# Kernel tuning notes

Measured on AMD Instinct MI355X. Metric: run time of the kernel, lower is better.

Reference implementation:

```python
import jax, jax.numpy as jnp
import numpy as np

B, S, D, H = 2, 2048, 1024, 16
HD = D // H
SCALE = float(np.sqrt(HD))


def setup_inputs() -> dict:
    key = jax.random.key(0)
    k_x, k_wqkv, k_bqkv, k_wo, k_bo = jax.random.split(key, 5)
    std = 1.0 / np.sqrt(D)
    x = jax.random.normal(k_x, (B, S, D), dtype=jnp.float32)
    mask = jnp.tril(jnp.ones((S, S), dtype=jnp.int32))[None, None]  # (1,1,S,S) causal
    W_qkv = jax.random.normal(k_wqkv, (D, 3 * D), dtype=jnp.float32) * std
    b_qkv = jax.random.normal(k_bqkv, (3 * D,), dtype=jnp.float32) * std
    W_o = jax.random.normal(k_wo, (D, D), dtype=jnp.float32) * std
    b_o = jax.random.normal(k_bo, (D,), dtype=jnp.float32) * std
    return {"x": x, "W_qkv": W_qkv, "b_qkv": b_qkv, "W_o": W_o, "b_o": b_o, "mask": mask}


def reference(x, W_qkv, b_qkv, W_o, b_o, mask):
    # fused QKV projection: (B,S,3D) -> (3,B,H,S,HD)
    qkv = x @ W_qkv + b_qkv
    qkv = qkv.reshape(B, S, 3, H, HD).transpose(2, 0, 3, 1, 4)
    Q, K, V = qkv[0], qkv[1], qkv[2]
    # scaled dot-product attention with explicit mask
    scores = jnp.einsum('bhqd,bhkd->bhqk', Q, K) / SCALE
    scores = jnp.where(mask == 0, -jnp.inf, scores)
    attn = jax.nn.softmax(scores, axis=-1)  # dropout p=0.0 -> identity
    context = jnp.einsum('bhqk,bhkd->bhqd', attn, V)
    context = context.transpose(0, 2, 1, 3).reshape(B, S, D)
    return context @ W_o + b_o
```

## Files before the change

### kernel.cpp

```cpp
#include <hip/hip_runtime.h>
#include <hip/hip_bf16.h>
#include <stdint.h>

#define DEV __device__ __forceinline__

typedef __bf16 bf16x8 __attribute__((ext_vector_type(8)));
typedef float f32x4 __attribute__((ext_vector_type(4)));
typedef float f32x16 __attribute__((ext_vector_type(16)));
typedef unsigned short ushort8 __attribute__((ext_vector_type(8)));

DEV uint16_t f2bf(float f) {
  uint32_t u = __float_as_uint(f);
  u += 0x7fffu + ((u >> 16) & 1u);
  return (uint16_t)(u >> 16);
}

DEV float exp2r(float x) {
  float r;
  asm("v_exp_f32 %0, %1" : "=v"(r) : "v"(x));
  return r;
}

DEV void gload_lds16(const void* g, void* l) {
  __builtin_amdgcn_global_load_lds(
      (const __attribute__((address_space(1))) void*)g,
      (__attribute__((address_space(3))) void*)l, 16, 0, 0);
}

DEV void swap32u(uint32_t& a, uint32_t& b) {
#if defined(__has_builtin) && __has_builtin(__builtin_amdgcn_permlane32_swap)
  auto r = __builtin_amdgcn_permlane32_swap(a, b, false, false);
  a = (uint32_t)r[0];
  b = (uint32_t)r[1];
#else
  uint32_t as = __shfl_xor(a, 32), bs = __shfl_xor(b, 32);
  uint32_t na = (threadIdx.x & 32) ? bs : a;
  uint32_t nb = (threadIdx.x & 32) ? b : as;
  a = na; b = nb;
#endif
}
DEV void swap32f(float& a, float& b) {
  uint32_t ua = __float_as_uint(a), ub = __float_as_uint(b);
  swap32u(ua, ub);
  a = __uint_as_float(ua); b = __uint_as_float(ub);
}

__global__ __launch_bounds__(256) void k_prep(const float* __restrict__ W0,
                                              uint16_t* __restrict__ WT0,
                                              const float* __restrict__ W1,
                                              uint16_t* __restrict__ WT1,
                                              const float* __restrict__ X,
                                              uint16_t* __restrict__ Xb) {
  const int z = blockIdx.z;
  const int tid = threadIdx.x;
  if (z == 2) {
    const int nt4 = 1048576, stride = 48 * 16 * 256;
    int base = (blockIdx.y * 48 + blockIdx.x) * 256 + tid;
    for (int i = base; i < nt4; i += stride) {
      float4 v = *reinterpret_cast<const float4*>(X + (size_t)i * 4);
      ushort4 o = { f2bf(v.x), f2bf(v.y), f2bf(v.z), f2bf(v.w) };
      *reinterpret_cast<ushort4*>(Xb + (size_t)i * 4) = o;
    }
    return;
  }
  if (z == 1 && blockIdx.x >= 16) return;
  const float* W = z ? W1 : W0;
  uint16_t* WT = z ? WT1 : WT0;
  const int K = 1024, N = z ? 1024 : 3072;
  __shared__ float t[64][65];
  int n0 = blockIdx.x * 64, k0 = blockIdx.y * 64;
  int r = tid >> 4, c4 = (tid & 15) * 4;
#pragma unroll
  for (int p = 0; p < 4; ++p) {
    int kr = p * 16 + r;
    float4 v = *reinterpret_cast<const float4*>(W + (size_t)(k0 + kr) * N + n0 + c4);
    t[kr][c4] = v.x; t[kr][c4 + 1] = v.y; t[kr][c4 + 2] = v.z; t[kr][c4 + 3] = v.w;
  }
  __syncthreads();
#pragma unroll
  for (int p = 0; p < 4; ++p) {
    int nr = p * 16 + r;
    ushort4 o = { f2bf(t[c4][nr]), f2bf(t[c4 + 1][nr]), f2bf(t[c4 + 2][nr]), f2bf(t[c4 + 3][nr]) };
    *reinterpret_cast<ushort4*>(WT + (size_t)(n0 + nr) * K + k0 + c4) = o;
  }
}

__global__ __launch_bounds__(256, 2) void k_gemm0(const uint16_t* __restrict__ A,
                                                  const uint16_t* __restrict__ Bw,
                                                  const float* __restrict__ bias,
                                                  uint16_t* __restrict__ o0,
                                                  uint16_t* __restrict__ o1,
                                                  uint16_t* __restrict__ o2) {
  constexpr int K = 1024;
  __shared__ __attribute__((aligned(16))) char SMEM[65536];
  const int tid = threadIdx.x;
  const int lane = tid & 63, wid = tid >> 6;
  const int g = lane >> 4, c = lane & 15;
  const int nb = gridDim.x * gridDim.y;
  const int bid = blockIdx.y * gridDim.x + blockIdx.x;
  const int cpx = nb >> 3;
  const int swz = (bid & 7) * cpx + (bid >> 3);
  const int bx = swz % gridDim.x, by = swz / gridDim.x;
  const int row0 = by * 128, col0 = bx * 128;
  const int wrow = (wid >> 1) * 64, wcol = (wid & 1) * 64;
  f32x4 acc[4][4] = {};
  const uint16_t* Ag = A + (size_t)row0 * K;
  const uint16_t* Bg = Bw + (size_t)col0 * K;

  const int srow = tid >> 3;
  const int ssw = ((tid & 7) ^ (srow & 7)) * 8;
  auto stageAB = [&](int t, int buf) {
    const int k0 = t * 64;
    char* ab = SMEM + buf * 16384;
    char* bb = SMEM + 32768 + buf * 16384;
#pragma unroll
    for (int i = 0; i < 4; ++i) {
      int row = i * 32 + srow;
      gload_lds16(Ag + (size_t)row * K + k0 + ssw, ab + i * 4096 + tid * 16);
      gload_lds16(Bg + (size_t)row * K + k0 + ssw, bb + i * 4096 + tid * 16);
    }
  };

  stageAB(0, 0);
  asm volatile("s_waitcnt vmcnt(0)" ::: "memory");
  __builtin_amdgcn_s_barrier();
  asm volatile("" ::: "memory");

  for (int t = 0; t < 16; ++t) {
    if (t + 1 < 16) stageAB(t + 1, (t + 1) & 1);
    const uint16_t* Ac = (const uint16_t*)(SMEM + (t & 1) * 16384);
    const uint16_t* Bc = (const uint16_t*)(SMEM + 32768 + (t & 1) * 16384);
    __builtin_amdgcn_s_setprio(1);
#pragma unroll
    for (int kk = 0; kk < 2; ++kk) {
      bf16x8 af[4], bf[4];
#pragma unroll
      for (int m = 0; m < 4; ++m)
        af[m] = *reinterpret_cast<const bf16x8*>(
            &Ac[(wrow + m * 16 + c) * 64 + (((kk * 4 + g) ^ (c & 7)) << 3)]);
#pragma unroll
      for (int n = 0; n < 4; ++n)
        bf[n] = *reinterpret_cast<const bf16x8*>(
            &Bc[(wcol + n * 16 + c) * 64 + (((kk * 4 + g) ^ (c & 7)) << 3)]);
#pragma unroll
      for (int m = 0; m < 4; ++m)
#pragma unroll
        for (int n = 0; n < 4; ++n)
          acc[m][n] = __builtin_amdgcn_mfma_f32_16x16x32_bf16(af[m], bf[n], acc[m][n], 0, 0, 0);
    }
    __builtin_amdgcn_s_setprio(0);
    asm volatile("s_waitcnt vmcnt(0)" ::: "memory");
    __builtin_amdgcn_s_barrier();
    asm volatile("" ::: "memory");
  }

  if (col0 >= 2048) {
    uint16_t* TB = (uint16_t*)SMEM;
#pragma unroll
    for (int n = 0; n < 4; ++n) {
      int col_l = wcol + n * 16 + c;
      float bs = bias[col0 + col_l];
#pragma unroll
      for (int m = 0; m < 4; ++m)
#pragma unroll
        for (int r = 0; r < 4; ++r) {
          int row_l = wrow + m * 16 + g * 4 + r;
          TB[col_l * 136 + row_l] = f2bf(acc[m][n][r] + bs);
        }
    }
    __syncthreads();
    const int col_l = tid >> 1, half = tid & 1;
    const int d = (col0 - 2048) + col_l;
    const int h = d >> 6, hd = d & 63;
    const int b = row0 >> 11, s0 = row0 & 2047;
    uint16_t* dst = o2 + ((size_t)(b * 16 + h) * 64 + hd) * 2048 + s0 + half * 64;
    const uint16_t* src = &TB[col_l * 136 + half * 64];
#pragma unroll
    for (int k = 0; k < 8; ++k) {
      ushort8 v = *reinterpret_cast<const ushort8*>(src + k * 8);
      *reinterpret_cast<ushort8*>(dst + k * 8) = v;
    }
  } else {
#pragma unroll
    for (int m = 0; m < 4; ++m) {
#pragma unroll
      for (int n = 0; n < 4; ++n) {
        int col = col0 + wcol + n * 16 + c;
        float bs = bias[col];
#pragma unroll
        for (int r = 0; r < 4; ++r) {
          int row = row0 + wrow + m * 16 + g * 4 + r;
          float v = acc[m][n][r] + bs;
          int which = col >> 10, d = col & 1023, h = d >> 6, hd = d & 63;
          int b = row >> 11, s = row & 2047;
          int bh = b * 16 + h;
          if (which == 0)      o0[((size_t)bh * 2048 + s) * 64 + hd] = f2bf(v * 0.1803368801111244f);
          else                 o1[((size_t)bh * 2048 + s) * 64 + hd] = f2bf(v);
        }
      }
    }
  }
}

__global__ __launch_bounds__(256, 2) void k_gemm1(const uint16_t* __restrict__ A,
                                                  const uint16_t* __restrict__ Bw,
                                                  const float* __restrict__ bias,
                                                  float* __restrict__ of) {
  constexpr int K = 1024;
  __shared__ __attribute__((aligned(16))) char SMEM[49152];
  const int tid = threadIdx.x;
  const int lane = tid & 63, wid = tid >> 6;
  const int g = lane >> 4, c = lane & 15;
  const int nb = gridDim.x * gridDim.y;
  const int bid = blockIdx.y * gridDim.x + blockIdx.x;
  const int cpx = nb >> 3;
  const int swz = (bid & 7) * cpx + (bid >> 3);
  const int bx = swz % gridDim.x, by = swz / gridDim.x;
  const int row0 = by * 128, col0 = bx * 64;
  f32x4 acc[2][4] = {};
  const uint16_t* Ag = A + (size_t)row0 * K;
  const uint16_t* Bg = Bw + (size_t)col0 * K;

  const int srow = tid >> 3;
  const int ssw = ((tid & 7) ^ (srow & 7)) * 8;
  auto stageAB = [&](int t, int buf) {
    const int k0 = t * 64;
    char* ab = SMEM + buf * 16384;
    char* bb = SMEM + 32768 + buf * 8192;
#pragma unroll
    for (int i = 0; i < 4; ++i)
      gload_lds16(Ag + (size_t)(i * 32 + srow) * K + k0 + ssw, ab + i * 4096 + tid * 16);
#pragma unroll
    for (int i = 0; i < 2; ++i)
      gload_lds16(Bg + (size_t)(i * 32 + srow) * K + k0 + ssw, bb + i * 4096 + tid * 16);
  };

  stageAB(0, 0);
  asm volatile("s_waitcnt vmcnt(0)" ::: "memory");
  __builtin_amdgcn_s_barrier();
  asm volatile("" ::: "memory");

  for (int t = 0; t < 16; ++t) {
    if (t + 1 < 16) stageAB(t + 1, (t + 1) & 1);
    const uint16_t* Ac = (const uint16_t*)(SMEM + (t & 1) * 16384);
    const uint16_t* Bc = (const uint16_t*)(SMEM + 32768 + (t & 1) * 8192);
    __builtin_amdgcn_s_setprio(1);
#pragma unroll
    for (int kk = 0; kk < 2; ++kk) {
      bf16x8 af[2], bf[4];
#pragma unroll
      for (int m = 0; m < 2; ++m)
        af[m] = *reinterpret_cast<const bf16x8*>(
            &Ac[(wid * 32 + m * 16 + c) * 64 + (((kk * 4 + g) ^ (c & 7)) << 3)]);
#pragma unroll
      for (int n = 0; n < 4; ++n)
        bf[n] = *reinterpret_cast<const bf16x8*>(
            &Bc[(n * 16 + c) * 64 + (((kk * 4 + g) ^ (c & 7)) << 3)]);
#pragma unroll
      for (int m = 0; m < 2; ++m)
#pragma unroll
        for (int n = 0; n < 4; ++n)
          acc[m][n] = __builtin_amdgcn_mfma_f32_16x16x32_bf16(af[m], bf[n], acc[m][n], 0, 0, 0);
    }
    __builtin_amdgcn_s_setprio(0);
    asm volatile("s_waitcnt vmcnt(0)" ::: "memory");
    __builtin_amdgcn_s_barrier();
    asm volatile("" ::: "memory");
  }

#pragma unroll
  for (int m = 0; m < 2; ++m) {
#pragma unroll
    for (int n = 0; n < 4; ++n) {
      int col = col0 + n * 16 + c;
      float bs = bias[col];
#pragma unroll
      for (int r = 0; r < 4; ++r) {
        int row = row0 + wid * 32 + m * 16 + g * 4 + r;
        of[(size_t)row * 1024 + col] = acc[m][n][r] + bs;
      }
    }
  }
}

__global__ __launch_bounds__(256, 2) void k_attn(const uint16_t* __restrict__ Qb,
                                                 const uint16_t* __restrict__ Kb,
                                                 const uint16_t* __restrict__ Vb,
                                                 uint16_t* __restrict__ ctx) {
  __shared__ __attribute__((aligned(16))) uint16_t Ks[2][128 * 64];
  __shared__ __attribute__((aligned(16))) uint16_t Vs[2][64 * 128];
  const int bid = blockIdx.x;
  const int xcd = bid & 7;
  const int idx = bid >> 3;
  const int bh = 4 * xcd + (idx & 3);
  const int jj = idx >> 2;
  const int qt = (idx < 32) ? (15 - jj) : (jj - 8);
  const int tid = threadIdx.x, lane = tid & 63, wid = tid >> 6;
  const int h2 = lane >> 5, c = lane & 31;
  const int q0 = qt * 128;
  const int qi = q0 + wid * 32 + c;
  const int nt = qt + 1;
  const uint16_t* Qh = Qb + (size_t)bh * 2048 * 64;
  const uint16_t* Kh = Kb + (size_t)bh * 2048 * 64;
  const uint16_t* Vh = Vb + (size_t)bh * 64 * 2048;

  bf16x8 qf[4];
#pragma unroll
  for (int kk = 0; kk < 4; ++kk)
    qf[kk] = *reinterpret_cast<const bf16x8*>(&Qh[(size_t)qi * 64 + kk * 16 + h2 * 8]);

  float m_ = -INFINITY, l_ = 0.f;
  f32x16 oT0 = {}, oT1 = {};

  const int srow = tid >> 3;
  const int ssw = ((tid & 7) ^ (srow & 7)) * 8;
  const int vr = tid >> 4;
  const int vsw = ((tid & 15) ^ vr) * 8;
  auto stage = [&](int T, int buf) {
    const int j0 = T * 128;
    char* kb = (char*)(&Ks[buf][0]);
    char* vb = (char*)(&Vs[buf][0]);
#pragma unroll
    for (int i = 0; i < 4; ++i)
      gload_lds16(Kh + (size_t)(j0 + i * 32 + srow) * 64 + ssw, kb + i * 4096 + tid * 16);
#pragma unroll
    for (int i = 0; i < 4; ++i)
      gload_lds16(Vh + (size_t)(i * 16 + vr) * 2048 + j0 + vsw, vb + i * 4096 + tid * 16);
  };

  union U4 { uint32_t u[4]; bf16x8 v; };

  stage(0, 0);
  asm volatile("s_waitcnt vmcnt(0)" ::: "memory");
  __builtin_amdgcn_s_barrier();
  asm volatile("" ::: "memory");

  for (int T = 0; T < nt; ++T) {
    const int j0 = T * 128;
    if (T + 1 < nt) stage(T + 1, (T + 1) & 1);
    const uint16_t* Kc = &Ks[T & 1][0];
    const uint16_t* Vc = &Vs[T & 1][0];
    f32x16 s0 = {}, s1 = {}, s2 = {}, s3 = {};
    __builtin_amdgcn_s_setprio(1);
#pragma unroll
    for (int kk = 0; kk < 4; ++kk) {
      const int off = ((kk * 2 + h2) ^ (c & 7)) << 3;
      bf16x8 k0 = *reinterpret_cast<const bf16x8*>(&Kc[(c) * 64 + off]);
      bf16x8 k1 = *reinterpret_cast<const bf16x8*>(&Kc[(32 + c) * 64 + off]);
      bf16x8 k2 = *reinterpret_cast<const bf16x8*>(&Kc[(64 + c) * 64 + off]);
      bf16x8 k3 = *reinterpret_cast<const bf16x8*>(&Kc[(96 + c) * 64 + off]);
      s0 = __builtin_amdgcn_mfma_f32_32x32x16_bf16(k0, qf[kk], s0, 0, 0, 0);
      s1 = __builtin_amdgcn_mfma_f32_32x32x16_bf16(k1, qf[kk], s1, 0, 0, 0);
      s2 = __builtin_amdgcn_mfma_f32_32x32x16_bf16(k2, qf[kk], s2, 0, 0, 0);
      s3 = __builtin_amdgcn_mfma_f32_32x32x16_bf16(k3, qf[kk], s3, 0, 0, 0);
    }
    __builtin_amdgcn_s_setprio(0);
    if (T == qt) {
#pragma unroll
      for (int r = 0; r < 16; ++r) {
        int key0 = j0 + (r & 3) + 8 * (r >> 2) + 4 * h2;
        if (key0 > qi) s0[r] = -INFINITY;
        if (key0 + 32 > qi) s1[r] = -INFINITY;
        if (key0 + 64 > qi) s2[r] = -INFINITY;
        if (key0 + 96 > qi) s3[r] = -INFINITY;
      }
    }
    float tm[16];
#pragma unroll
    for (int r = 0; r < 16; ++r)
      tm[r] = fmaxf(fmaxf(s0[r], s1[r]), fmaxf(s2[r], s3[r]));
#pragma unroll
    for (int s = 8; s >= 1; s >>= 1)
#pragma unroll
      for (int r = 0; r < s; ++r) tm[r] = fmaxf(tm[r], tm[r + s]);
    float xa = tm[0], xb = tm[0];
    swap32f(xa, xb);
    float mx = fmaxf(xa, xb);
    bool nogrow = __all(mx <= m_ + 8.0f) != 0;
    float nm = m_, scl = 1.0f;
    if (!nogrow) { nm = fmaxf(m_, mx); scl = exp2r(m_ - nm); m_ = nm; }
    float sum = 0.f;
    uint32_t W[32];
#pragma unroll
    for (int w = 0; w < 8; ++w) {
      float a0 = exp2r(s0[2 * w] - nm), a1 = exp2r(s0[2 * w + 1] - nm);
      float b0 = exp2r(s1[2 * w] - nm), b1 = exp2r(s1[2 * w + 1] - nm);
      float c0 = exp2r(s2[2 * w] - nm), c1 = exp2r(s2[2 * w + 1] - nm);
      float d0 = exp2r(s3[2 * w] - nm), d1 = exp2r(s3[2 * w + 1] - nm);
      sum += ((a0 + a1) + (b0 + b1)) + ((c0 + c1) + (d0 + d1));
      asm("v_cvt_pk_bf16_f32 %0, %1, %2" : "=v"(W[w])      : "v"(a0), "v"(a1));
      asm("v_cvt_pk_bf16_f32 %0, %1, %2" : "=v"(W[8 + w])  : "v"(b0), "v"(b1));
      asm("v_cvt_pk_bf16_f32 %0, %1, %2" : "=v"(W[16 + w]) : "v"(c0), "v"(c1));
      asm("v_cvt_pk_bf16_f32 %0, %1, %2" : "=v"(W[24 + w]) : "v"(d0), "v"(d1));
    }
    float sa = sum, sb = sum;
    swap32f(sa, sb);
    sum = sa + sb;
    l_ = l_ * scl + sum;
    if (!nogrow) {
#pragma unroll
      for (int r = 0; r < 16; ++r) { oT0[r] *= scl; oT1[r] *= scl; }
    }
#pragma unroll
    for (int ch = 0; ch < 4; ++ch) {
      uint32_t* Wc = &W[ch * 8];
      U4 p0, p1;
      uint32_t a0 = Wc[0], b0 = Wc[2];  swap32u(a0, b0);
      uint32_t a1 = Wc[1], b1 = Wc[3];  swap32u(a1, b1);
      p0.u[0] = a0; p0.u[1] = a1; p0.u[2] = b0; p0.u[3] = b1;
      uint32_t a2 = Wc[4], b2 = Wc[6];  swap32u(a2, b2);
      uint32_t a3 = Wc[5], b3 = Wc[7];  swap32u(a3, b3);
      p1.u[0] = a2; p1.u[1] = a3; p1.u[2] = b2; p1.u[3] = b3;
      const int cb = ch * 4 + h2;
      const int vsl0 = (cb ^ (c & 15)) << 3;
      const int vsl1 = (((cb + 2) & 15) ^ (c & 15)) << 3;
      __builtin_amdgcn_s_setprio(1);
      {
        bf16x8 v0 = *reinterpret_cast<const bf16x8*>(&Vc[c * 128 + vsl0]);
        bf16x8 v1 = *reinterpret_cast<const bf16x8*>(&Vc[c * 128 + vsl1]);
        oT0 = __builtin_amdgcn_mfma_f32_32x32x16_bf16(v0, p0.v, oT0, 0, 0, 0);
        oT0 = __builtin_amdgcn_mfma_f32_32x32x16_bf16(v1, p1.v, oT0, 0, 0, 0);
      }
      {
        bf16x8 v0 = *reinterpret_cast<const bf16x8*>(&Vc[(32 + c) * 128 + vsl0]);
        bf16x8 v1 = *reinterpret_cast<const bf16x8*>(&Vc[(32 + c) * 128 + vsl1]);
        oT1 = __builtin_amdgcn_mfma_f32_32x32x16_bf16(v0, p0.v, oT1, 0, 0, 0);
        oT1 = __builtin_amdgcn_mfma_f32_32x32x16_bf16(v1, p1.v, oT1, 0, 0, 0);
      }
      __builtin_amdgcn_s_setprio(0);
    }
    asm volatile("s_waitcnt vmcnt(0)" ::: "memory");
    __builtin_amdgcn_s_barrier();
    asm volatile("" ::: "memory");
  }

  const int b = bh >> 4, h = bh & 15;
  float inv = 1.0f / l_;
  int token = b * 2048 + qi;
  uint16_t* outp = ctx + (size_t)token * 1024 + h * 64;
#pragma unroll
  for (int hb = 0; hb < 2; ++hb) {
    const f32x16& o = hb ? oT1 : oT0;
#pragma unroll
    for (int q4 = 0; q4 < 4; ++q4) {
      ushort4 w;
      w.x = f2bf(o[q4 * 4 + 0] * inv);
      w.y = f2bf(o[q4 * 4 + 1] * inv);
      w.z = f2bf(o[q4 * 4 + 2] * inv);
      w.w = f2bf(o[q4 * 4 + 3] * inv);
      *reinterpret_cast<ushort4*>(outp + hb * 32 + 8 * q4 + 4 * h2) = w;
    }
  }
}

extern "C" void kernel_launch(void* const* d_in, const int* in_sizes, int n_in,
                              void* d_out, int out_size, void* d_ws, size_t ws_size,
                              hipStream_t stream) {
  (void)in_sizes; (void)n_in; (void)out_size; (void)ws_size;
  const float* x     = (const float*)d_in[0];
  const float* W_qkv = (const float*)d_in[1];
  const float* b_qkv = (const float*)d_in[2];
  const float* W_o   = (const float*)d_in[3];
  const float* b_o   = (const float*)d_in[4];
  uint16_t* ws    = (uint16_t*)d_ws;
  uint16_t* xb    = ws;
  uint16_t* wqkvT = xb + 4096 * 1024;
  uint16_t* woT   = wqkvT + 3072 * 1024;
  uint16_t* Qb    = woT + 1024 * 1024;
  uint16_t* Kb    = Qb + 32 * 2048 * 64;
  uint16_t* Vb    = Kb + 32 * 2048 * 64;
  uint16_t* ctx   = Vb + 32 * 2048 * 64;

  k_prep<<<dim3(48, 16, 3), 256, 0, stream>>>(W_qkv, wqkvT, W_o, woT, x, xb);
  k_gemm0<<<dim3(24, 32), 256, 0, stream>>>(xb, wqkvT, b_qkv, Qb, Kb, Vb);
  k_attn<<<512, 256, 0, stream>>>(Qb, Kb, Vb, ctx);
  k_gemm1<<<dim3(16, 32), 256, 0, stream>>>(ctx, woT, b_o, (float*)d_out);
}
```

Baseline: 96.39 us.

## Split long causal query tiles across two blocks and merge partial softmax results

The six longest causal query tiles (qt 10-15) are each split into two KV ranges handled by separate blocks, which write unnormalized partial outputs plus running max and sum to scratch. A new merge kernel combines the two halves with log-sum-exp rescaling. A constant table schedules the 704 blocks so work is balanced across CUs and the long-tail imbalance of causal attention shrinks. The cost is an extra kernel launch, fp32 partial traffic, and reuse of the xb workspace region (the workspace layout is reordered so that region is free) as scratch.

```diff
diff --git a/kernel.cpp b/kernel.cpp
--- a/kernel.cpp
+++ b/kernel.cpp
@@ -44,6 +44,13 @@
   swap32u(ua, ub);
   a = __uint_as_float(ua); b = __uint_as_float(ub);
 }
+
+__constant__ int QT_TAB[22] = {9, 8, 15, 15, 14, 7, 14, 13, 13, 12, 6,
+                               12, 11, 11, 10, 5, 10, 4, 3, 2, 1, 0};
+__constant__ int T0_TAB[22] = {0, 0, 0, 8, 0, 0, 8, 0, 7, 0, 0,
+                               7, 0, 6, 0, 0, 6, 0, 0, 0, 0, 0};
+__constant__ int T1_TAB[22] = {10, 9, 8, 16, 8, 8, 15, 7, 14, 7, 7,
+                               13, 6, 12, 6, 6, 11, 5, 4, 3, 2, 1};
 
 __global__ __launch_bounds__(256) void k_prep(const float* __restrict__ W0,
                                               uint16_t* __restrict__ WT0,
@@ -286,20 +293,22 @@
 __global__ __launch_bounds__(256, 2) void k_attn(const uint16_t* __restrict__ Qb,
                                                  const uint16_t* __restrict__ Kb,
                                                  const uint16_t* __restrict__ Vb,
-                                                 uint16_t* __restrict__ ctx) {
+                                                 uint16_t* __restrict__ ctx,
+                                                 float* __restrict__ PO,
+                                                 float* __restrict__ PML) {
   __shared__ __attribute__((aligned(16))) uint16_t Ks[2][128 * 64];
   __shared__ __attribute__((aligned(16))) uint16_t Vs[2][64 * 128];
   const int bid = blockIdx.x;
   const int xcd = bid & 7;
   const int idx = bid >> 3;
   const int bh = 4 * xcd + (idx & 3);
-  const int jj = idx >> 2;
-  const int qt = (idx < 32) ? (15 - jj) : (jj - 8);
+  const int j = idx >> 2;
+  const int qt = QT_TAB[j];
+  const int T0 = T0_TAB[j], T1 = T1_TAB[j];
   const int tid = threadIdx.x, lane = tid & 63, wid = tid >> 6;
   const int h2 = lane >> 5, c = lane & 31;
   const int q0 = qt * 128;
   const int qi = q0 + wid * 32 + c;
-  const int nt = qt + 1;
   const uint16_t* Qh = Qb + (size_t)bh * 2048 * 64;
   const uint16_t* Kh = Kb + (size_t)bh * 2048 * 64;
   const uint16_t* Vh = Vb + (size_t)bh * 64 * 2048;
@@ -330,16 +339,17 @@
 
   union U4 { uint32_t u[4]; bf16x8 v; };
 
-  stage(0, 0);
+  stage(T0, 0);
   asm volatile("s_waitcnt vmcnt(0)" ::: "memory");
   __builtin_amdgcn_s_barrier();
   asm volatile("" ::: "memory");
 
-  for (int T = 0; T < nt; ++T) {
+  for (int T = T0; T < T1; ++T) {
     const int j0 = T * 128;
-    if (T + 1 < nt) stage(T + 1, (T + 1) & 1);
-    const uint16_t* Kc = &Ks[T & 1][0];
-    const uint16_t* Vc = &Vs[T & 1][0];
+    const int buf = (T - T0) & 1;
+    if (T + 1 < T1) stage(T + 1, buf ^ 1);
+    const uint16_t* Kc = &Ks[buf][0];
+    const uint16_t* Vc = &Vs[buf][0];
     f32x16 s0 = {}, s1 = {}, s2 = {}, s3 = {};
     __builtin_amdgcn_s_setprio(1);
 #pragma unroll
@@ -434,22 +444,73 @@
     asm volatile("" ::: "memory");
   }
 
+  if (qt < 10) {
+    const int b = bh >> 4, h = bh & 15;
+    float inv = 1.0f / l_;
+    int token = b * 2048 + qi;
+    uint16_t* outp = ctx + (size_t)token * 1024 + h * 64;
+#pragma unroll
+    for (int hb = 0; hb < 2; ++hb) {
+      const f32x16& o = hb ? oT1 : oT0;
+#pragma unroll
+      for (int q4 = 0; q4 < 4; ++q4) {
+        ushort4 w;
+        w.x = f2bf(o[q4 * 4 + 0] * inv);
+        w.y = f2bf(o[q4 * 4 + 1] * inv);
+        w.z = f2bf(o[q4 * 4 + 2] * inv);
+        w.w = f2bf(o[q4 * 4 + 3] * inv);
+        *reinterpret_cast<ushort4*>(outp + hb * 32 + 8 * q4 + 4 * h2) = w;
+      }
+    }
+  } else {
+    const int half = (T0 != 0) ? 1 : 0;
+    const int slot = (bh * 6 + (qt - 10)) * 2 + half;
+    float* po = PO + (size_t)slot * 8192;
+    float* pml = PML + (size_t)slot * 256;
+    const int row_l = wid * 32 + c;
+    pml[row_l * 2] = m_;
+    pml[row_l * 2 + 1] = l_;
+#pragma unroll
+    for (int hb = 0; hb < 2; ++hb) {
+      const f32x16& o = hb ? oT1 : oT0;
+#pragma unroll
+      for (int q4 = 0; q4 < 4; ++q4) {
+        float4 w = { o[q4 * 4 + 0], o[q4 * 4 + 1], o[q4 * 4 + 2], o[q4 * 4 + 3] };
+        *reinterpret_cast<float4*>(po + row_l * 64 + hb * 32 + 8 * q4 + 4 * h2) = w;
+      }
+    }
+  }
+}
+
+__global__ __launch_bounds__(256) void k_merge(const float* __restrict__ PO,
+                                               const float* __restrict__ PML,
+                                               uint16_t* __restrict__ ctx) {
+  const int bid = blockIdx.x;
+  const int bh = bid & 31, pi = bid >> 5;
+  const int qt = 10 + pi;
+  const int slot0 = (bh * 6 + pi) * 2;
+  const float* poL = PO + (size_t)slot0 * 8192;
+  const float* poH = poL + 8192;
+  const float* mlL = PML + (size_t)slot0 * 256;
+  const float* mlH = mlL + 256;
+  const int t = threadIdx.x;
+  const int r = t >> 1, ho = (t & 1) * 32;
+  float mL = mlL[r * 2], lL = mlL[r * 2 + 1];
+  float mH = mlH[r * 2], lH = mlH[r * 2 + 1];
+  float m = fmaxf(mL, mH);
+  float eL = exp2f(mL - m), eH = exp2f(mH - m);
+  float inv = 1.0f / (lL * eL + lH * eH);
+  float sL = eL * inv, sH = eH * inv;
   const int b = bh >> 4, h = bh & 15;
-  float inv = 1.0f / l_;
-  int token = b * 2048 + qi;
-  uint16_t* outp = ctx + (size_t)token * 1024 + h * 64;
-#pragma unroll
-  for (int hb = 0; hb < 2; ++hb) {
-    const f32x16& o = hb ? oT1 : oT0;
-#pragma unroll
-    for (int q4 = 0; q4 < 4; ++q4) {
-      ushort4 w;
-      w.x = f2bf(o[q4 * 4 + 0] * inv);
-      w.y = f2bf(o[q4 * 4 + 1] * inv);
-      w.z = f2bf(o[q4 * 4 + 2] * inv);
-      w.w = f2bf(o[q4 * 4 + 3] * inv);
-      *reinterpret_cast<ushort4*>(outp + hb * 32 + 8 * q4 + 4 * h2) = w;
-    }
+  const int token = b * 2048 + qt * 128 + r;
+  uint16_t* outp = ctx + (size_t)token * 1024 + h * 64 + ho;
+#pragma unroll
+  for (int k4 = 0; k4 < 8; ++k4) {
+    float4 a = *reinterpret_cast<const float4*>(poL + r * 64 + ho + k4 * 4);
+    float4 q = *reinterpret_cast<const float4*>(poH + r * 64 + ho + k4 * 4);
+    ushort4 w = { f2bf(a.x * sL + q.x * sH), f2bf(a.y * sL + q.y * sH),
+                  f2bf(a.z * sL + q.z * sH), f2bf(a.w * sL + q.w * sH) };
+    *reinterpret_cast<ushort4*>(outp + k4 * 4) = w;
   }
 }
 
@@ -463,16 +524,19 @@
   const float* W_o   = (const float*)d_in[3];
   const float* b_o   = (const float*)d_in[4];
   uint16_t* ws    = (uint16_t*)d_ws;
-  uint16_t* xb    = ws;
+  uint16_t* woT   = ws;
+  uint16_t* xb    = woT + 1024 * 1024;
   uint16_t* wqkvT = xb + 4096 * 1024;
-  uint16_t* woT   = wqkvT + 3072 * 1024;
-  uint16_t* Qb    = woT + 1024 * 1024;
+  uint16_t* Qb    = wqkvT + 3072 * 1024;
   uint16_t* Kb    = Qb + 32 * 2048 * 64;
   uint16_t* Vb    = Kb + 32 * 2048 * 64;
   uint16_t* ctx   = Vb + 32 * 2048 * 64;
+  float* PO  = (float*)xb;
+  float* PML = PO + 384 * 8192;
 
   k_prep<<<dim3(48, 16, 3), 256, 0, stream>>>(W_qkv, wqkvT, W_o, woT, x, xb);
   k_gemm0<<<dim3(24, 32), 256, 0, stream>>>(xb, wqkvT, b_qkv, Qb, Kb, Vb);
-  k_attn<<<512, 256, 0, stream>>>(Qb, Kb, Vb, ctx);
+  k_attn<<<704, 256, 0, stream>>>(Qb, Kb, Vb, ctx, PO, PML);
+  k_merge<<<192, 256, 0, stream>>>(PO, PML, ctx);
   k_gemm1<<<dim3(16, 32), 256, 0, stream>>>(ctx, woT, b_o, (float*)d_out);
 }
```

Result: slower. 99.03 us (+2.7%).

## Split attention key tiles across two wave groups and merge softmax partials

Applied to the files above, without the earlier changes.

The attention kernel now runs 512 threads per block. Eight waves split each 128-key tile into two 64-key halves, so each wave keeps only two score accumulators instead of four. Each half keeps its own online-softmax max, sum and output. At the end the two partials are merged through shared memory and written once. This is meant to cut per-wave register pressure and serial work per tile and raise occupancy, at the cost of a final merge step and a barrier. The workspace layout is also reordered.

```diff
diff --git a/kernel.cpp b/kernel.cpp
--- a/kernel.cpp
+++ b/kernel.cpp
@@ -283,12 +283,13 @@
   }
 }
 
-__global__ __launch_bounds__(256, 2) void k_attn(const uint16_t* __restrict__ Qb,
+__global__ __launch_bounds__(512, 4) void k_attn(const uint16_t* __restrict__ Qb,
                                                  const uint16_t* __restrict__ Kb,
                                                  const uint16_t* __restrict__ Vb,
                                                  uint16_t* __restrict__ ctx) {
-  __shared__ __attribute__((aligned(16))) uint16_t Ks[2][128 * 64];
-  __shared__ __attribute__((aligned(16))) uint16_t Vs[2][64 * 128];
+  __shared__ __attribute__((aligned(16))) char SMEM[65536];
+  uint16_t* Ksb = (uint16_t*)SMEM;
+  uint16_t* Vsb = (uint16_t*)(SMEM + 32768);
   const int bid = blockIdx.x;
   const int xcd = bid & 7;
   const int idx = bid >> 3;
@@ -296,9 +297,10 @@
   const int jj = idx >> 2;
   const int qt = (idx < 32) ? (15 - jj) : (jj - 8);
   const int tid = threadIdx.x, lane = tid & 63, wid = tid >> 6;
+  const int qw = wid & 3, kw = wid >> 2;
   const int h2 = lane >> 5, c = lane & 31;
   const int q0 = qt * 128;
-  const int qi = q0 + wid * 32 + c;
+  const int qi = q0 + qw * 32 + c;
   const int nt = qt + 1;
   const uint16_t* Qh = Qb + (size_t)bh * 2048 * 64;
   const uint16_t* Kh = Kb + (size_t)bh * 2048 * 64;
@@ -309,23 +311,23 @@
   for (int kk = 0; kk < 4; ++kk)
     qf[kk] = *reinterpret_cast<const bf16x8*>(&Qh[(size_t)qi * 64 + kk * 16 + h2 * 8]);
 
-  float m_ = -INFINITY, l_ = 0.f;
+  float m_ = -1e30f, l_ = 0.f;
   f32x16 oT0 = {}, oT1 = {};
 
   const int srow = tid >> 3;
   const int ssw = ((tid & 7) ^ (srow & 7)) * 8;
   const int vr = tid >> 4;
-  const int vsw = ((tid & 15) ^ vr) * 8;
+  const int vsw = ((tid & 15) ^ (vr & 15)) * 8;
   auto stage = [&](int T, int buf) {
     const int j0 = T * 128;
-    char* kb = (char*)(&Ks[buf][0]);
-    char* vb = (char*)(&Vs[buf][0]);
-#pragma unroll
-    for (int i = 0; i < 4; ++i)
-      gload_lds16(Kh + (size_t)(j0 + i * 32 + srow) * 64 + ssw, kb + i * 4096 + tid * 16);
-#pragma unroll
-    for (int i = 0; i < 4; ++i)
-      gload_lds16(Vh + (size_t)(i * 16 + vr) * 2048 + j0 + vsw, vb + i * 4096 + tid * 16);
+    char* kb = (char*)(Ksb + buf * 8192);
+    char* vb = (char*)(Vsb + buf * 8192);
+#pragma unroll
+    for (int i = 0; i < 2; ++i)
+      gload_lds16(Kh + (size_t)(j0 + i * 64 + srow) * 64 + ssw, kb + i * 8192 + tid * 16);
+#pragma unroll
+    for (int i = 0; i < 2; ++i)
+      gload_lds16(Vh + (size_t)(i * 32 + vr) * 2048 + j0 + vsw, vb + i * 8192 + tid * 16);
   };
 
   union U4 { uint32_t u[4]; bf16x8 v; };
@@ -338,37 +340,31 @@
   for (int T = 0; T < nt; ++T) {
     const int j0 = T * 128;
     if (T + 1 < nt) stage(T + 1, (T + 1) & 1);
-    const uint16_t* Kc = &Ks[T & 1][0];
-    const uint16_t* Vc = &Vs[T & 1][0];
-    f32x16 s0 = {}, s1 = {}, s2 = {}, s3 = {};
+    const uint16_t* Kc = Ksb + (T & 1) * 8192;
+    const uint16_t* Vc = Vsb + (T & 1) * 8192;
+    f32x16 s0 = {}, s1 = {};
     __builtin_amdgcn_s_setprio(1);
 #pragma unroll
     for (int kk = 0; kk < 4; ++kk) {
       const int off = ((kk * 2 + h2) ^ (c & 7)) << 3;
-      bf16x8 k0 = *reinterpret_cast<const bf16x8*>(&Kc[(c) * 64 + off]);
-      bf16x8 k1 = *reinterpret_cast<const bf16x8*>(&Kc[(32 + c) * 64 + off]);
-      bf16x8 k2 = *reinterpret_cast<const bf16x8*>(&Kc[(64 + c) * 64 + off]);
-      bf16x8 k3 = *reinterpret_cast<const bf16x8*>(&Kc[(96 + c) * 64 + off]);
+      bf16x8 k0 = *reinterpret_cast<const bf16x8*>(&Kc[(kw * 64 + c) * 64 + off]);
+      bf16x8 k1 = *reinterpret_cast<const bf16x8*>(&Kc[(kw * 64 + 32 + c) * 64 + off]);
       s0 = __builtin_amdgcn_mfma_f32_32x32x16_bf16(k0, qf[kk], s0, 0, 0, 0);
       s1 = __builtin_amdgcn_mfma_f32_32x32x16_bf16(k1, qf[kk], s1, 0, 0, 0);
-      s2 = __builtin_amdgcn_mfma_f32_32x32x16_bf16(k2, qf[kk], s2, 0, 0, 0);
-      s3 = __builtin_amdgcn_mfma_f32_32x32x16_bf16(k3, qf[kk], s3, 0, 0, 0);
     }
     __builtin_amdgcn_s_setprio(0);
     if (T == qt) {
 #pragma unroll
       for (int r = 0; r < 16; ++r) {
-        int key0 = j0 + (r & 3) + 8 * (r >> 2) + 4 * h2;
+        int key0 = j0 + kw * 64 + (r & 3) + 8 * (r >> 2) + 4 * h2;
         if (key0 > qi) s0[r] = -INFINITY;
         if (key0 + 32 > qi) s1[r] = -INFINITY;
-        if (key0 + 64 > qi) s2[r] = -INFINITY;
-        if (key0 + 96 > qi) s3[r] = -INFINITY;
       }
     }
     float tm[16];
 #pragma unroll
     for (int r = 0; r < 16; ++r)
-      tm[r] = fmaxf(fmaxf(s0[r], s1[r]), fmaxf(s2[r], s3[r]));
+      tm[r] = fmaxf(s0[r], s1[r]);
 #pragma unroll
     for (int s = 8; s >= 1; s >>= 1)
 #pragma unroll
@@ -380,18 +376,14 @@
     float nm = m_, scl = 1.0f;
     if (!nogrow) { nm = fmaxf(m_, mx); scl = exp2r(m_ - nm); m_ = nm; }
     float sum = 0.f;
-    uint32_t W[32];
+    uint32_t W[16];
 #pragma unroll
     for (int w = 0; w < 8; ++w) {
       float a0 = exp2r(s0[2 * w] - nm), a1 = exp2r(s0[2 * w + 1] - nm);
       float b0 = exp2r(s1[2 * w] - nm), b1 = exp2r(s1[2 * w + 1] - nm);
-      float c0 = exp2r(s2[2 * w] - nm), c1 = exp2r(s2[2 * w + 1] - nm);
-      float d0 = exp2r(s3[2 * w] - nm), d1 = exp2r(s3[2 * w + 1] - nm);
-      sum += ((a0 + a1) + (b0 + b1)) + ((c0 + c1) + (d0 + d1));
-      asm("v_cvt_pk_bf16_f32 %0, %1, %2" : "=v"(W[w])      : "v"(a0), "v"(a1));
-      asm("v_cvt_pk_bf16_f32 %0, %1, %2" : "=v"(W[8 + w])  : "v"(b0), "v"(b1));
-      asm("v_cvt_pk_bf16_f32 %0, %1, %2" : "=v"(W[16 + w]) : "v"(c0), "v"(c1));
-      asm("v_cvt_pk_bf16_f32 %0, %1, %2" : "=v"(W[24 + w]) : "v"(d0), "v"(d1));
+      sum += (a0 + a1) + (b0 + b1);
+      asm("v_cvt_pk_bf16_f32 %0, %1, %2" : "=v"(W[w])     : "v"(a0), "v"(a1));
+      asm("v_cvt_pk_bf16_f32 %0, %1, %2" : "=v"(W[8 + w]) : "v"(b0), "v"(b1));
     }
     float sa = sum, sb = sum;
     swap32f(sa, sb);
@@ -402,8 +394,8 @@
       for (int r = 0; r < 16; ++r) { oT0[r] *= scl; oT1[r] *= scl; }
     }
 #pragma unroll
-    for (int ch = 0; ch < 4; ++ch) {
-      uint32_t* Wc = &W[ch * 8];
+    for (int cc = 0; cc < 2; ++cc) {
+      uint32_t* Wc = &W[cc * 8];
       U4 p0, p1;
       uint32_t a0 = Wc[0], b0 = Wc[2];  swap32u(a0, b0);
       uint32_t a1 = Wc[1], b1 = Wc[3];  swap32u(a1, b1);
@@ -411,7 +403,7 @@
       uint32_t a2 = Wc[4], b2 = Wc[6];  swap32u(a2, b2);
       uint32_t a3 = Wc[5], b3 = Wc[7];  swap32u(a3, b3);
       p1.u[0] = a2; p1.u[1] = a3; p1.u[2] = b2; p1.u[3] = b3;
-      const int cb = ch * 4 + h2;
+      const int cb = (kw * 2 + cc) * 4 + h2;
       const int vsl0 = (cb ^ (c & 15)) << 3;
       const int vsl1 = (((cb + 2) & 15) ^ (c & 15)) << 3;
       __builtin_amdgcn_s_setprio(1);
@@ -434,21 +426,39 @@
     asm volatile("" ::: "memory");
   }
 
-  const int b = bh >> 4, h = bh & 15;
-  float inv = 1.0f / l_;
-  int token = b * 2048 + qi;
-  uint16_t* outp = ctx + (size_t)token * 1024 + h * 64;
-#pragma unroll
-  for (int hb = 0; hb < 2; ++hb) {
-    const f32x16& o = hb ? oT1 : oT0;
-#pragma unroll
-    for (int q4 = 0; q4 < 4; ++q4) {
-      ushort4 w;
-      w.x = f2bf(o[q4 * 4 + 0] * inv);
-      w.y = f2bf(o[q4 * 4 + 1] * inv);
-      w.z = f2bf(o[q4 * 4 + 2] * inv);
-      w.w = f2bf(o[q4 * 4 + 3] * inv);
-      *reinterpret_cast<ushort4*>(outp + hb * 32 + 8 * q4 + 4 * h2) = w;
+  float* MB = (float*)SMEM;
+  float* OB = MB + 512;
+  const int sl = qw * 64 + lane;
+  if (kw == 1) {
+    MB[sl * 2] = m_;
+    MB[sl * 2 + 1] = l_;
+    float* ob = OB + sl * 33;
+#pragma unroll
+    for (int r = 0; r < 16; ++r) { ob[r] = oT0[r]; ob[16 + r] = oT1[r]; }
+  }
+  __syncthreads();
+  if (kw == 0) {
+    float mB = MB[sl * 2], lB = MB[sl * 2 + 1];
+    const float* ob = OB + sl * 33;
+    float m = fmaxf(m_, mB);
+    float eA = exp2r(m_ - m), eB = exp2r(mB - m);
+    float inv = 1.0f / (l_ * eA + lB * eB);
+    float sA = eA * inv, sB = eB * inv;
+    const int b = bh >> 4, h = bh & 15;
+    int token = b * 2048 + qi;
+    uint16_t* outp = ctx + (size_t)token * 1024 + h * 64;
+#pragma unroll
+    for (int hb = 0; hb < 2; ++hb) {
+      const f32x16& o = hb ? oT1 : oT0;
+#pragma unroll
+      for (int q4 = 0; q4 < 4; ++q4) {
+        ushort4 w;
+        w.x = f2bf(o[q4 * 4 + 0] * sA + ob[hb * 16 + q4 * 4 + 0] * sB);
+        w.y = f2bf(o[q4 * 4 + 1] * sA + ob[hb * 16 + q4 * 4 + 1] * sB);
+        w.z = f2bf(o[q4 * 4 + 2] * sA + ob[hb * 16 + q4 * 4 + 2] * sB);
+        w.w = f2bf(o[q4 * 4 + 3] * sA + ob[hb * 16 + q4 * 4 + 3] * sB);
+        *reinterpret_cast<ushort4*>(outp + hb * 32 + 8 * q4 + 4 * h2) = w;
+      }
     }
   }
 }
@@ -463,16 +473,16 @@
   const float* W_o   = (const float*)d_in[3];
   const float* b_o   = (const float*)d_in[4];
   uint16_t* ws    = (uint16_t*)d_ws;
-  uint16_t* xb    = ws;
+  uint16_t* woT   = ws;
+  uint16_t* xb    = woT + 1024 * 1024;
   uint16_t* wqkvT = xb + 4096 * 1024;
-  uint16_t* woT   = wqkvT + 3072 * 1024;
-  uint16_t* Qb    = woT + 1024 * 1024;
+  uint16_t* Qb    = wqkvT + 3072 * 1024;
   uint16_t* Kb    = Qb + 32 * 2048 * 64;
   uint16_t* Vb    = Kb + 32 * 2048 * 64;
   uint16_t* ctx   = Vb + 32 * 2048 * 64;
 
   k_prep<<<dim3(48, 16, 3), 256, 0, stream>>>(W_qkv, wqkvT, W_o, woT, x, xb);
   k_gemm0<<<dim3(24, 32), 256, 0, stream>>>(xb, wqkvT, b_qkv, Qb, Kb, Vb);
-  k_attn<<<512, 256, 0, stream>>>(Qb, Kb, Vb, ctx);
+  k_attn<<<512, 512, 0, stream>>>(Qb, Kb, Vb, ctx);
   k_gemm1<<<dim3(16, 32), 256, 0, stream>>>(ctx, woT, b_o, (float*)d_out);
 }
```

Result: faster. 91.36 us (-5.2%).
